# Kernel tuning notes

Hardware: AMD Instinct MI355X
Metric: run time of the kernel (lower is better)

Reference implementation:

```python
import jax, jax.numpy as jnp
import numpy as np


def _conv1x1(t, W, b):
    # 1x1 conv == per-pixel channel GEMM: [B,C,H,W] x [O,C] -> [B,O,H,W]
    return jnp.einsum('bchw,oc->bohw', t, W) + b[None, :, None, None]


def setup_inputs() -> dict:
    key = jax.random.key(0)
    ks = jax.random.split(key, 10)
    B, C, H, W = 8, 256, 96, 96
    s = 1.0 / np.sqrt(C)
    inp = {
        'x': jax.random.normal(ks[0], (B, C, H, W), dtype=jnp.float32),
        'Wq': jax.random.normal(ks[1], (C, C), dtype=jnp.float32) * s,
        'bq': jax.random.normal(ks[2], (C,), dtype=jnp.float32) * 0.01,
        'Wk': jax.random.normal(ks[3], (C, C), dtype=jnp.float32) * s,
        'bk': jax.random.normal(ks[4], (C,), dtype=jnp.float32) * 0.01,
        'Wv': jax.random.normal(ks[5], (C, C), dtype=jnp.float32) * s,
        'bv': jax.random.normal(ks[6], (C,), dtype=jnp.float32) * 0.01,
        'Ws': jax.random.normal(ks[7], (C, C), dtype=jnp.float32) * s,
        'bs': jax.random.normal(ks[8], (C,), dtype=jnp.float32) * 0.01,
        # torch init is zeros; use a nonzero scalar so the attention branch matters
        'gamma': jax.random.normal(ks[9], (1,), dtype=jnp.float32) * 0.5,
    }
    return inp


def reference(x, Wq, bq, Wk, bk, Wv, bv, Ws, bs, gamma):
    B, C, H, W = x.shape
    N = H * W
    # query: [B, N, C]
    q = _conv1x1(x, Wq, bq).reshape(B, C, N).transpose(0, 2, 1)
    # key: 1x1 conv, then stride-3 1x1 conv (== subsample every 3rd pixel, then GEMM)
    k = _conv1x1(x, Wk, bk)
    k = _conv1x1(k[:, :, ::3, ::3], Ws, bs)
    Ns = k.shape[2] * k.shape[3]
    k = k.reshape(B, C, Ns)
    energy = jnp.einsum('bnc,bcm->bnm', q, k)       # [B, N, Ns]
    attn = jax.nn.softmax(energy, axis=-1)
    # value: same 1x1 conv + strided 1x1 conv pipeline
    v = _conv1x1(x, Wv, bv)
    v = _conv1x1(v[:, :, ::3, ::3], Ws, bs).reshape(B, C, Ns)
    out = jnp.einsum('bcm,bnm->bcn', v, attn).reshape(B, C, H, W)
    return gamma[0] * out + x
```

## Files before the change

### kernel.cpp

```cpp
#include <hip/hip_runtime.h>

typedef _Float16 f16;
typedef _Float16 f16x8 __attribute__((ext_vector_type(8)));
typedef __fp16 fp16x2 __attribute__((ext_vector_type(2)));
typedef float f32x4 __attribute__((ext_vector_type(4)));
typedef float f32x16 __attribute__((ext_vector_type(16)));

#define CDIM 256
#define NPIX 9216
#define NB 8

__device__ __forceinline__ f32x4 mfma16(f16x8 a, f16x8 b, f32x4 c) {
  return __builtin_amdgcn_mfma_f32_16x16x32_f16(a, b, c, 0, 0, 0);
}
__device__ __forceinline__ f32x16 mfma32(f16x8 a, f16x8 b, f32x16 c) {
  return __builtin_amdgcn_mfma_f32_32x32x16_f16(a, b, c, 0, 0, 0);
}
__device__ __forceinline__ f16x8 ld8(const f16* p) { return *(const f16x8*)p; }

__device__ __forceinline__ void stage16(const void* g, void* l) {
  __builtin_amdgcn_global_load_lds((const __attribute__((address_space(1))) unsigned int*)g,
                                   (__attribute__((address_space(3))) unsigned int*)l, 16, 0, 0);
}
#define S_BARRIER() do { asm volatile("" ::: "memory"); __builtin_amdgcn_s_barrier(); asm volatile("" ::: "memory"); } while (0)
#define WAIT_VM(N) do { asm volatile("s_waitcnt vmcnt(" #N ")" ::: "memory"); __builtin_amdgcn_sched_barrier(0); } while (0)

__device__ __forceinline__ unsigned pkrtz(float a, float b) {
  union { fp16x2 h; unsigned u; } cv;
  cv.h = __builtin_amdgcn_cvt_pkrtz(a, b);
  return cv.u;
}
union U8 { f16x8 v; unsigned u[4]; };

__device__ __forceinline__ f16x8 pack_swap(float v0, float v1, float v2, float v3,
                                           float v4, float v5, float v6, float v7,
                                           int hh) {
  unsigned a  = pkrtz(v0, v1);
  unsigned b2 = pkrtz(v2, v3);
  unsigned c2 = pkrtz(v4, v5);
  unsigned d2 = pkrtz(v6, v7);
  unsigned ex1 = __shfl_xor(hh ? a : c2, 32);
  unsigned ex2 = __shfl_xor(hh ? b2 : d2, 32);
  U8 r;
  r.u[0] = hh ? ex1 : a;
  r.u[1] = hh ? ex2 : b2;
  r.u[2] = hh ? c2 : ex1;
  r.u[3] = hh ? d2 : ex2;
  return r.v;
}


__global__ void prep_weights(const float* __restrict__ Wq,
                             const float* __restrict__ Wk, const float* __restrict__ bk,
                             const float* __restrict__ Wv, const float* __restrict__ bv,
                             const float* __restrict__ Ws, const float* __restrict__ bs,
                             f16* __restrict__ WqF, f16* __restrict__ WkF, f16* __restrict__ WvF,
                             float* __restrict__ bk2, float* __restrict__ bv2) {
  int o = blockIdx.x, c = threadIdx.x;
  float ak = 0.f, av = 0.f;
  for (int i = 0; i < CDIM; ++i) {
    float w = Ws[o*CDIM + i];
    ak += w * Wk[i*CDIM + c];
    av += w * Wv[i*CDIM + c];
  }
  {
    size_t qbyte = (size_t)((o >> 5)*16 + (c >> 4))*1024
                 + (size_t)(((c >> 3) & 1)*32 + (o & 31))*16 + (c & 7)*2;
    *(f16*)((char*)WqF + qbyte) = (f16)Wq[o*CDIM + c];
    size_t fbyte = (size_t)((o >> 4)*8 + (c >> 5))*1024
                 + (size_t)(16*((c >> 3) & 3) + (o & 15))*16 + (c & 7)*2;
    *(f16*)((char*)WkF + fbyte) = (f16)ak;
    *(f16*)((char*)WvF + fbyte) = (f16)av;
  }
  if (c == 0) {
    float sk = 0.f, sv = 0.f;
    for (int i = 0; i < CDIM; ++i) { float w = Ws[o*CDIM + i]; sk += w*bk[i]; sv += w*bv[i]; }
    bk2[o] = sk + bs[o];
    bv2[o] = sv + bs[o];
  }
}

__global__ void transpose_x(const float* __restrict__ x, char* __restrict__ xT) {
  __shared__ f16 tile[32][34];
  int c0 = blockIdx.x * 32, n0 = blockIdx.y * 32, b = blockIdx.z;
  int tx = threadIdx.x, ty = threadIdx.y;
#pragma unroll
  for (int j = 0; j < 4; ++j) {
    int cl = ty + 8*j;
    tile[cl][tx] = (f16)x[(size_t)(b*CDIM + c0 + cl)*NPIX + n0 + tx];
  }
  __syncthreads();
  int tid = ty*32 + tx;
  if (tid < 128) {
    int nl = tid >> 2, u = tid & 3;
    int n = n0 + nl;
    int cu = (c0 >> 3) + u;
    f16x8 v;
#pragma unroll
    for (int e = 0; e < 8; ++e) v[e] = tile[8*u + e][nl];
    size_t byte = (size_t)(b*NPIX + n)*512 + (size_t)((cu ^ (n & 7)) << 4);
    *(f16x8*)(xT + byte) = v;
  }
}

__global__ __launch_bounds__(256) void compute_kv(
    const char* __restrict__ xT, const f16* __restrict__ WkF, const f16* __restrict__ WvF,
    const float* __restrict__ bk2, const float* __restrict__ bv2,
    char* __restrict__ kB, char* __restrict__ vB) {
  int ch = blockIdx.x;
  int m0 = ch * 32;
  int b = blockIdx.y;
  int tid = threadIdx.x;
  int w = tid >> 6, lane = tid & 63, l15 = lane & 15, q = lane >> 4;
  size_t chbase = (size_t)(b*32 + ch)*16384;

  const char* xrow[2]; int xn7[2];
#pragma unroll
  for (int mt2 = 0; mt2 < 2; ++mt2) {
    int m = m0 + 16*mt2 + l15;
    int n = 288*(m >> 5) + 3*(m & 31);
    xrow[mt2] = xT + (size_t)(b*NPIX + n)*512;
    xn7[mt2] = n & 7;
  }
  const char* wkf = (const char*)WkF + (size_t)lane*16;
  const char* wvf = (const char*)WvF + (size_t)lane*16;

  f32x4 accK[2][4] = {};
  f32x4 accV[4][2] = {};
  for (int ks = 0; ks < 8; ++ks) {
    f16x8 am[2], wk[4], wv[4];
#pragma unroll
    for (int mt2 = 0; mt2 < 2; ++mt2)
      am[mt2] = *(const f16x8*)(xrow[mt2] + (((q + 4*ks) ^ xn7[mt2]) << 4));
#pragma unroll
    for (int t = 0; t < 4; ++t) {
      wk[t] = *(const f16x8*)(wkf + (size_t)((4*w + t)*8 + ks)*1024);
      wv[t] = *(const f16x8*)(wvf + (size_t)((4*w + t)*8 + ks)*1024);
    }
#pragma unroll
    for (int mt2 = 0; mt2 < 2; ++mt2)
#pragma unroll
      for (int ot = 0; ot < 4; ++ot) {
        accK[mt2][ot] = mfma16(am[mt2], wk[ot], accK[mt2][ot]);
        accV[ot][mt2] = mfma16(wv[ot], am[mt2], accV[ot][mt2]);
      }
  }
#pragma unroll
  for (int mt2 = 0; mt2 < 2; ++mt2)
#pragma unroll
    for (int ot = 0; ot < 4; ++ot) {
      int cin = 64*w + 16*ot + l15;
      float bo = bk2[cin];
      size_t fb = chbase + (size_t)(cin >> 4)*1024 + (size_t)(((cin >> 3) & 1)*32)*16 + (cin & 7)*2;
#pragma unroll
      for (int r = 0; r < 4; ++r) {
        int keyrel = 16*mt2 + 4*q + r;
        *(f16*)(kB + fb + (size_t)keyrel*16) = (f16)(accK[mt2][ot][r] + bo);
      }
    }
#pragma unroll
  for (int ct = 0; ct < 4; ++ct) {
    f32x4 bv4 = *(const f32x4*)(bv2 + 64*w + 16*ct + 4*q);
#pragma unroll
    for (int mt2 = 0; mt2 < 2; ++mt2) {
#pragma unroll
      for (int r = 0; r < 4; ++r) {
        int c = 64*w + 16*ct + 4*q + r;
        size_t byte = chbase + (size_t)(2*(c >> 5) + mt2)*1024
                    + (size_t)((l15 >> 3)*32 + (c & 31))*16 + (l15 & 7)*2;
        *(f16*)(vB + byte) = (f16)(accV[ct][mt2][r] + bv4[r]);
      }
    }
  }
}

__global__ __launch_bounds__(256, 2) void attention(
    const char* __restrict__ xT, const f16* __restrict__ WqF, const float* __restrict__ bq,
    const char* __restrict__ kB, const char* __restrict__ vB,
    const float* __restrict__ xg, const float* __restrict__ gamma_p,
    float* __restrict__ out) {
  __shared__ char lds[65536];

  int bid = blockIdx.x;
  int b = bid & 7;
  int tile = bid >> 3;
  int tid = threadIdx.x;
  int w = tid >> 6, lane = tid & 63, l31 = lane & 31, hh = lane >> 5;
  int n0w = tile*128 + w*32;
  int lane16 = lane * 16;

  const char* kBb = kB + (size_t)b*524288;
  const char* vBb = vB + (size_t)b*524288;

  {
    int so = tid * 16;
#pragma unroll
    for (int r = 0; r < 4; ++r) stage16(kBb + so + r*4096, lds + so + r*4096);
#pragma unroll
    for (int r = 0; r < 4; ++r) stage16(vBb + so + r*4096, lds + 16384 + so + r*4096);
  }

  f16x8 qf[16];
  {
    f16x8 xb[16];
    int n = n0w + l31;
    const char* xrow = xT + (size_t)(b*NPIX + n)*512;
    int n7 = n & 7;
#pragma unroll
    for (int s = 0; s < 16; ++s)
      xb[s] = *(const f16x8*)(xrow + (((2*s + hh) ^ n7) << 4));
#pragma unroll
    for (int ot = 0; ot < 8; ++ot) {
      f32x16 acc;
#pragma unroll
      for (int j = 0; j < 16; ++j) acc[j] = 0.f;
#pragma unroll
      for (int s = 0; s < 16; ++s) {
        f16x8 wa = *(const f16x8*)((const char*)WqF + (size_t)(ot*16 + s)*1024 + lane16);
        acc = mfma32(wa, xb[s], acc);
      }
#pragma unroll
      for (int i = 0; i < 4; ++i) {
        f32x4 bv4 = *(const f32x4*)(bq + 32*ot + 8*i + 4*hh);
#pragma unroll
        for (int j2 = 0; j2 < 4; ++j2) acc[4*i + j2] += bv4[j2];
      }
      qf[2*ot + 0] = pack_swap(acc[0], acc[1], acc[2], acc[3],
                               acc[4], acc[5], acc[6], acc[7], hh);
      qf[2*ot + 1] = pack_swap(acc[8], acc[9], acc[10], acc[11],
                               acc[12], acc[13], acc[14], acc[15], hh);
    }
  }

  f32x16 O[8];
#pragma unroll
  for (int i = 0; i < 8; ++i)
#pragma unroll
    for (int j = 0; j < 16; ++j) O[i][j] = 0.f;
  float m_run = -3e38f, l_run = 0.f;

  for (int t = 0; t < 32; ++t) {
    char* curb = lds + ((t & 1) << 15);
    if (t < 31) {
      const char* ksrc = kBb + (size_t)(t + 1)*16384;
      const char* vsrc = vBb + (size_t)(t + 1)*16384;
      char* kd = lds + (((t + 1) & 1) << 15);
      int so = tid * 16;
#pragma unroll
      for (int r = 0; r < 4; ++r) stage16(ksrc + so + r*4096, kd + so + r*4096);
#pragma unroll
      for (int r = 0; r < 4; ++r) stage16(vsrc + so + r*4096, kd + 16384 + so + r*4096);
      WAIT_VM(8);
    } else {
      WAIT_VM(0);
    }
    S_BARRIER();

    f32x16 SA, SB;
#pragma unroll
    for (int j = 0; j < 16; ++j) { SA[j] = 0.f; SB[j] = 0.f; }
    __builtin_amdgcn_s_setprio(1);
#pragma unroll
    for (int s = 0; s < 8; ++s) {
      f16x8 kfa = *(const f16x8*)(curb + (2*s)*1024 + lane16);
      SA = mfma32(kfa, qf[2*s], SA);
      f16x8 kfb = *(const f16x8*)(curb + (2*s + 1)*1024 + lane16);
      SB = mfma32(kfb, qf[2*s + 1], SB);
    }
    __builtin_amdgcn_s_setprio(0);
    f32x16 S16;
#pragma unroll
    for (int j = 0; j < 16; ++j) S16[j] = SA[j] + SB[j];

    float mx = S16[0];
#pragma unroll
    for (int j = 1; j < 16; ++j) mx = fmaxf(mx, S16[j]);
    mx = fmaxf(mx, __shfl_xor(mx, 32));
    if (!__all(mx <= m_run + 8.0f)) {
      float mn = fmaxf(m_run, mx);
      float al = __expf(m_run - mn);
      m_run = mn;
      l_run *= al;
#pragma unroll
      for (int i = 0; i < 8; ++i)
#pragma unroll
        for (int j = 0; j < 16; ++j) O[i][j] *= al;
    }
    float p[16];
    float ls = 0.f;
#pragma unroll
    for (int j = 0; j < 16; ++j) { p[j] = __expf(S16[j] - m_run); ls += p[j]; }
    l_run += ls;

    f16x8 pf0 = pack_swap(p[0], p[1], p[2], p[3], p[4], p[5], p[6], p[7], hh);
    f16x8 pf1 = pack_swap(p[8], p[9], p[10], p[11], p[12], p[13], p[14], p[15], hh);

    __builtin_amdgcn_s_setprio(1);
#pragma unroll
    for (int ct = 0; ct < 8; ++ct) {
      f16x8 vf0 = *(const f16x8*)(curb + 16384 + (ct*2 + 0)*1024 + lane16);
      O[ct] = mfma32(vf0, pf0, O[ct]);
      f16x8 vf1 = *(const f16x8*)(curb + 16384 + (ct*2 + 1)*1024 + lane16);
      O[ct] = mfma32(vf1, pf1, O[ct]);
    }
    __builtin_amdgcn_s_setprio(0);
    S_BARRIER();
  }

  l_run += __shfl_xor(l_run, 32);
  float inv = 1.0f / l_run;
  float g = gamma_p[0];
  int n = n0w + l31;
#pragma unroll
  for (int ct = 0; ct < 8; ++ct)
#pragma unroll
    for (int j = 0; j < 16; ++j) {
      int c = 32*ct + (j & 3) + 8*(j >> 2) + 4*hh;
      size_t idx = (size_t)(b*CDIM + c)*NPIX + n;
      out[idx] = g * (O[ct][j] * inv) + xg[idx];
    }
}

extern "C" void kernel_launch(void* const* d_in, const int* in_sizes, int n_in,
                              void* d_out, int out_size, void* d_ws, size_t ws_size,
                              hipStream_t stream) {
  (void)in_sizes; (void)n_in; (void)out_size; (void)ws_size;
  const float* x     = (const float*)d_in[0];
  const float* Wq    = (const float*)d_in[1];
  const float* bq    = (const float*)d_in[2];
  const float* Wk    = (const float*)d_in[3];
  const float* bk    = (const float*)d_in[4];
  const float* Wv    = (const float*)d_in[5];
  const float* bv    = (const float*)d_in[6];
  const float* Ws    = (const float*)d_in[7];
  const float* bs    = (const float*)d_in[8];
  const float* gamma = (const float*)d_in[9];

  char* ws = (char*)d_ws;
  float* bk2 = (float*)(ws);
  float* bv2 = (float*)(ws + 1024);
  char* xT   = ws + 4096;
  char* kB   = ws + 4096 + 37748736;
  char* vB   = kB + 4194304;
  f16* WqF   = (f16*)(vB + 4194304);
  f16* WkF   = WqF + 65536;
  f16* WvF   = WkF + 65536;

  prep_weights<<<256, 256, 0, stream>>>(Wq, Wk, bk, Wv, bv, Ws, bs, WqF, WkF, WvF, bk2, bv2);
  transpose_x<<<dim3(8, 288, 8), dim3(32, 8), 0, stream>>>(x, xT);
  compute_kv<<<dim3(32, 8), 256, 0, stream>>>(xT, WkF, WvF, bk2, bv2, kB, vB);
  attention<<<576, 256, 0, stream>>>(xT, WqF, bq, kB, vB, x, gamma, (float*)d_out);
}
```

Before: 195.1 us.

## Fuse weight prep and x transpose into one launch with larger tiles

Merges the weight-folding kernel and the x transpose kernel into a single launch: the first 256 blocks fold the weights and the remaining 1152 blocks transpose x. Each transpose block now covers 64 pixels across all 256 channels in a loop instead of one 32x32 tile. The goal is to remove one kernel launch, let weight prep overlap with the transpose, and cut the per-block overhead of the transpose. In exchange, each transpose block runs serially through 8 channel tiles with two barriers each, and the whole grid shares the larger shared-memory tile.

```diff
diff --git a/kernel.cpp b/kernel.cpp
--- a/kernel.cpp
+++ b/kernel.cpp
@@ -50,20 +50,23 @@
 }
 
 
-__global__ void prep_weights(const float* __restrict__ Wq,
-                             const float* __restrict__ Wk, const float* __restrict__ bk,
-                             const float* __restrict__ Wv, const float* __restrict__ bv,
-                             const float* __restrict__ Ws, const float* __restrict__ bs,
-                             f16* __restrict__ WqF, f16* __restrict__ WkF, f16* __restrict__ WvF,
-                             float* __restrict__ bk2, float* __restrict__ bv2) {
-  int o = blockIdx.x, c = threadIdx.x;
-  float ak = 0.f, av = 0.f;
-  for (int i = 0; i < CDIM; ++i) {
-    float w = Ws[o*CDIM + i];
-    ak += w * Wk[i*CDIM + c];
-    av += w * Wv[i*CDIM + c];
-  }
-  {
+__global__ __launch_bounds__(256) void prep_and_transpose(
+    const float* __restrict__ x, char* __restrict__ xT,
+    const float* __restrict__ Wq,
+    const float* __restrict__ Wk, const float* __restrict__ bk,
+    const float* __restrict__ Wv, const float* __restrict__ bv,
+    const float* __restrict__ Ws, const float* __restrict__ bs,
+    f16* __restrict__ WqF, f16* __restrict__ WkF, f16* __restrict__ WvF,
+    float* __restrict__ bk2, float* __restrict__ bv2) {
+  __shared__ f16 tile[32][66];
+  if (blockIdx.x < 256) {
+    int o = blockIdx.x, c = threadIdx.x;
+    float ak = 0.f, av = 0.f;
+    for (int i = 0; i < CDIM; ++i) {
+      float w = Ws[o*CDIM + i];
+      ak += w * Wk[i*CDIM + c];
+      av += w * Wv[i*CDIM + c];
+    }
     size_t qbyte = (size_t)((o >> 5)*16 + (c >> 4))*1024
                  + (size_t)(((c >> 3) & 1)*32 + (o & 31))*16 + (c & 7)*2;
     *(f16*)((char*)WqF + qbyte) = (f16)Wq[o*CDIM + c];
@@ -71,35 +74,37 @@
                  + (size_t)(16*((c >> 3) & 3) + (o & 15))*16 + (c & 7)*2;
     *(f16*)((char*)WkF + fbyte) = (f16)ak;
     *(f16*)((char*)WvF + fbyte) = (f16)av;
-  }
-  if (c == 0) {
-    float sk = 0.f, sv = 0.f;
-    for (int i = 0; i < CDIM; ++i) { float w = Ws[o*CDIM + i]; sk += w*bk[i]; sv += w*bv[i]; }
-    bk2[o] = sk + bs[o];
-    bv2[o] = sv + bs[o];
-  }
-}
-
-__global__ void transpose_x(const float* __restrict__ x, char* __restrict__ xT) {
-  __shared__ f16 tile[32][34];
-  int c0 = blockIdx.x * 32, n0 = blockIdx.y * 32, b = blockIdx.z;
-  int tx = threadIdx.x, ty = threadIdx.y;
-#pragma unroll
-  for (int j = 0; j < 4; ++j) {
-    int cl = ty + 8*j;
-    tile[cl][tx] = (f16)x[(size_t)(b*CDIM + c0 + cl)*NPIX + n0 + tx];
-  }
-  __syncthreads();
-  int tid = ty*32 + tx;
-  if (tid < 128) {
-    int nl = tid >> 2, u = tid & 3;
-    int n = n0 + nl;
-    int cu = (c0 >> 3) + u;
-    f16x8 v;
-#pragma unroll
-    for (int e = 0; e < 8; ++e) v[e] = tile[8*u + e][nl];
-    size_t byte = (size_t)(b*NPIX + n)*512 + (size_t)((cu ^ (n & 7)) << 4);
-    *(f16x8*)(xT + byte) = v;
+    if (c == 0) {
+      float sk = 0.f, sv = 0.f;
+      for (int i = 0; i < CDIM; ++i) { float w = Ws[o*CDIM + i]; sk += w*bk[i]; sv += w*bv[i]; }
+      bk2[o] = sk + bs[o];
+      bv2[o] = sv + bs[o];
+    }
+  } else {
+    int idx = blockIdx.x - 256;
+    int b = idx / 144;
+    int n0 = (idx % 144) * 64;
+    int tid = threadIdx.x;
+    int px = tid & 63, ch4 = tid >> 6;
+    int row = tid >> 2, u = tid & 3;
+    int n = n0 + row;
+    size_t outrow = (size_t)(b*NPIX + n)*512;
+#pragma unroll 1
+    for (int ct = 0; ct < 8; ++ct) {
+      int c0 = ct * 32;
+#pragma unroll
+      for (int j = 0; j < 8; ++j) {
+        int cl = ch4 + 4*j;
+        tile[cl][px] = (f16)x[(size_t)(b*CDIM + c0 + cl)*NPIX + n0 + px];
+      }
+      __syncthreads();
+      f16x8 v;
+#pragma unroll
+      for (int e = 0; e < 8; ++e) v[e] = tile[8*u + e][row];
+      int cu = ct*4 + u;
+      *(f16x8*)(xT + outrow + (size_t)((cu ^ (n & 7)) << 4)) = v;
+      __syncthreads();
+    }
   }
 }
 
@@ -346,8 +351,8 @@
   f16* WkF   = WqF + 65536;
   f16* WvF   = WkF + 65536;
 
-  prep_weights<<<256, 256, 0, stream>>>(Wq, Wk, bk, Wv, bv, Ws, bs, WqF, WkF, WvF, bk2, bv2);
-  transpose_x<<<dim3(8, 288, 8), dim3(32, 8), 0, stream>>>(x, xT);
+  prep_and_transpose<<<1408, 256, 0, stream>>>(x, xT, Wq, Wk, bk, Wv, bv, Ws, bs,
+                                               WqF, WkF, WvF, bk2, bv2);
   compute_kv<<<dim3(32, 8), 256, 0, stream>>>(xT, WkF, WvF, bk2, bv2, kB, vB);
   attention<<<576, 256, 0, stream>>>(xT, WqF, bq, kB, vB, x, gamma, (float*)d_out);
 }
```

New measurement: 188.1 us. 3.6% less time.
